# Performance work log

Hardware: AMD Instinct MI355X
Metric: run time of the kernel (lower is better)

Reference implementation:

```python
import jax, jax.numpy as jnp
import numpy as np

BLANK_ID = 0
B, MAX_T, MAX_U, VOCAB = 4, 200, 101, 1024  # MAX_U = max_label_len + 1


def setup_inputs() -> dict:
    key = jax.random.key(0)
    k1, k2, k3 = jax.random.split(key, 3)
    logits = jax.random.normal(k1, (B, MAX_T, MAX_U, VOCAB), dtype=jnp.float32)
    labels = jax.random.randint(k2, (B, MAX_U - 1), 0, VOCAB).astype(jnp.int64)
    label_lengths = jax.random.randint(k3, (B,), 1, MAX_U).astype(jnp.int64)  # in [1, MAX_U-1]
    attention_mask = jnp.ones((B, MAX_T), dtype=jnp.int32)
    return {"logits": logits, "labels": labels,
            "label_lengths": label_lengths, "attention_mask": attention_mask}


def _alpha_lattice(blank_lp, label_lp):
    """Forward variables for one sample.

    blank_lp: [T, U]   log P(blank | t, u)
    label_lp: [T, U-1] log P(y_u | t, u)  (label emitted at grid column u)
    Returns alpha [T, U], matching the reference recursion:
      alpha[0,0]   = blank_lp[0,0]
      alpha[t,0]   = alpha[t-1,0] + blank_lp[t,0]
      alpha[0,u]   = alpha[0,u-1] + label_lp[0,u-1]
      alpha[t,u]   = logaddexp(alpha[t-1,u]+blank_lp[t,u], alpha[t,u-1]+label_lp[t,u-1])
    """
    # First row: pure label path (cumulative sum along u).
    row0 = blank_lp[0, 0] + jnp.concatenate(
        [jnp.zeros((1,), blank_lp.dtype), jnp.cumsum(label_lp[0])])

    def time_step(prev_row, xs):
        b_t, l_t = xs                 # [U], [U-1]
        from_blank = prev_row + b_t   # blank transition into row t

        def u_step(carry, x):
            bl, lb = x
            a = jnp.logaddexp(bl, carry + lb)
            return a, a

        _, rest = jax.lax.scan(u_step, from_blank[0], (from_blank[1:], l_t))
        row = jnp.concatenate([from_blank[:1], rest])
        return row, row

    _, rows = jax.lax.scan(time_step, row0, (blank_lp[1:], label_lp[1:]))
    return jnp.concatenate([row0[None], rows], axis=0)  # [T, U]


def reference(logits, labels, label_lengths, attention_mask):
    Bn, maxT, maxU, V = logits.shape
    input_lengths = jnp.clip(attention_mask.sum(axis=1).astype(jnp.int32), 1, maxT)
    lab_lens = jnp.clip(label_lengths.astype(jnp.int32), 0, maxU - 1)
    labels_c = jnp.clip(labels, 0, V - 1)

    lp = jax.nn.log_softmax(logits, axis=-1)          # [B, T, U, V]
    blank_lp = lp[..., BLANK_ID]                      # [B, T, U]
    # label_lp[b, t, u] = lp[b, t, u, labels[b, u]] for u in [0, U-2]
    idx = jnp.broadcast_to(labels_c[:, None, :, None], (Bn, maxT, maxU - 1, 1))
    label_lp = jnp.take_along_axis(lp[:, :, :-1, :], idx, axis=3)[..., 0]

    alpha = jax.vmap(_alpha_lattice)(blank_lp, label_lp)  # [B, T, U]

    t_idx = input_lengths - 1
    u_idx = lab_lens                                  # U_b - 1 = label_len
    loss_b = -alpha[jnp.arange(Bn), t_idx, u_idx]

    valid = (input_lengths > 0) & (lab_lens > 0)
    loss_b = jnp.where(valid, loss_b, 0.0)
    num_valid = jnp.maximum(valid.sum(), 1)
    return loss_b.sum() / num_valid                   # reduction='mean'
```

## Files before the change

### kernel.cpp

```cpp
#include <hip/hip_runtime.h>
#include <hip/hip_bf16.h>
#include <math.h>

#define BB 4
#define TT 200
#define UU 101
#define VV 1024
#define NCELL (BB*TT*UU)

__device__ __forceinline__ float f4max(const float4& v) {
    return fmaxf(fmaxf(v.x, v.y), fmaxf(v.z, v.w));
}
__device__ __forceinline__ float f4comp(const float4& v, int c) {
    switch (c & 3) { case 0: return v.x; case 1: return v.y; case 2: return v.z; default: return v.w; }
}

__global__ __launch_bounds__(256) void lse_kernel(
        const float* __restrict__ logits,
        const int*   __restrict__ labels,
        float* __restrict__ blank_lp,
        float* __restrict__ label_lp) {
    const int wave = threadIdx.x >> 6;
    const int lane = threadIdx.x & 63;
    const int cell = blockIdx.x * 4 + wave;
    if (cell >= NCELL) return;
    const int b   = cell / (TT * UU);
    const int rem = cell % (TT * UU);
    const int t   = rem / UU;
    const int u   = rem % UU;

    const float4* src = (const float4*)(logits + (size_t)cell * VV);
    float4 x0 = src[lane];
    float4 x1 = src[lane + 64];
    float4 x2 = src[lane + 128];
    float4 x3 = src[lane + 192];

    float m = fmaxf(fmaxf(f4max(x0), f4max(x1)), fmaxf(f4max(x2), f4max(x3)));
    #pragma unroll
    for (int off = 32; off; off >>= 1) m = fmaxf(m, __shfl_xor(m, off));

    float s = 0.f;
    s += __expf(x0.x - m) + __expf(x0.y - m) + __expf(x0.z - m) + __expf(x0.w - m);
    s += __expf(x1.x - m) + __expf(x1.y - m) + __expf(x1.z - m) + __expf(x1.w - m);
    s += __expf(x2.x - m) + __expf(x2.y - m) + __expf(x2.z - m) + __expf(x2.w - m);
    s += __expf(x3.x - m) + __expf(x3.y - m) + __expf(x3.z - m) + __expf(x3.w - m);
    #pragma unroll
    for (int off = 32; off; off >>= 1) s += __shfl_xor(s, off);

    const float lse = m + __logf(s);

    if (lane == 0) blank_lp[cell] = x0.x - lse;

    if (u < UU - 1) {
        int l = labels[b * (UU - 1) + u];
        l = min(max(l, 0), VV - 1);
        const int lane_l = (l >> 2) & 63;
        if (lane == lane_l) {
            const int j = l >> 8;
            const int c = l & 3;
            float val = (j == 0) ? f4comp(x0, c) : (j == 1) ? f4comp(x1, c)
                      : (j == 2) ? f4comp(x2, c) : f4comp(x3, c);
            label_lp[(b * TT + t) * (UU - 1) + u] = val - lse;
        }
    }
}

__global__ __launch_bounds__(128) void alpha_kernel(
        const float* __restrict__ blank_lp,
        const float* __restrict__ label_lp,
        const int*   __restrict__ lab_lens,
        const int*   __restrict__ attn,
        float* __restrict__ loss_b,
        int*   __restrict__ valid_b) {
    const int b = blockIdx.x;
    const int u = threadIdx.x;

    __shared__ float buf[2][UU];
    __shared__ int   s_part[2];
    __shared__ float s_loss;

    int acc = 0;
    for (int i = threadIdx.x; i < TT; i += 128) acc += attn[b * TT + i];
    #pragma unroll
    for (int off = 32; off; off >>= 1) acc += __shfl_xor(acc, off);
    if ((threadIdx.x & 63) == 0) s_part[threadIdx.x >> 6] = acc;
    __syncthreads();
    int inlen = s_part[0] + s_part[1];
    inlen = min(max(inlen, 1), TT);
    const int tmax = inlen - 1;
    int lab = lab_lens[b];
    lab = min(max(lab, 0), UU - 1);
    const int ndiag = tmax + lab + 1;

    const float* bl_base = blank_lp + b * TT * UU;
    const float* lb_base = label_lp + b * TT * (UU - 1);
    const int um = min(u, UU - 1);
    const int ul = (um >= 1) ? (um - 1) : 0;

    auto fetch = [&](int d, float& fb, float& fl) {
        int tc = d - u;
        tc = min(max(tc, 0), TT - 1);
        fb = bl_base[tc * UU + um];
        fl = lb_base[tc * (UU - 1) + ul];
    };

    float cb[4], cl[4], nb[4], nl[4];
    #pragma unroll
    for (int k = 0; k < 4; ++k) fetch(k, cb[k], cl[k]);

    const int ng = (ndiag + 3) >> 2;
    for (int g = 0; g < ng; ++g) {
        const int dbase = g * 4;
        #pragma unroll
        for (int k = 0; k < 4; ++k) fetch(dbase + 4 + k, nb[k], nl[k]);
        #pragma unroll
        for (int k = 0; k < 4; ++k) {
            const int d = dbase + k;
            if (d < ndiag) {
                const int t = d - u;
                const bool act = (u <= lab) && (t >= 0) && (t <= tmax);
                if (act) {
                    const float fb = cb[k], fl = cl[k];
                    float v;
                    if (d == 0) {
                        v = fb;
                    } else if (u == 0) {
                        v = buf[(d - 1) & 1][0] + fb;
                    } else if (t == 0) {
                        v = buf[(d - 1) & 1][u - 1] + fl;
                    } else {
                        const float a = buf[(d - 1) & 1][u] + fb;
                        const float c = buf[(d - 1) & 1][u - 1] + fl;
                        const float mx = fmaxf(a, c), mn = fminf(a, c);
                        v = mx + log1pf(__expf(mn - mx));
                    }
                    buf[d & 1][u] = v;
                    if (t == tmax && u == lab) s_loss = -v;
                }
            }
            __syncthreads();
        }
        #pragma unroll
        for (int k = 0; k < 4; ++k) { cb[k] = nb[k]; cl[k] = nl[k]; }
    }

    if (threadIdx.x == 0) {
        loss_b[b]  = s_loss;
        valid_b[b] = (lab > 0) ? 1 : 0;
    }
}

__global__ void finalize_kernel(const float* __restrict__ loss_b,
                                const int* __restrict__ valid_b,
                                float* __restrict__ out) {
    if (threadIdx.x == 0 && blockIdx.x == 0) {
        float s = 0.f;
        int nv = 0;
        for (int b = 0; b < BB; ++b) {
            if (valid_b[b]) { s += loss_b[b]; ++nv; }
        }
        out[0] = s / (float)max(nv, 1);
    }
}

extern "C" void kernel_launch(void* const* d_in, const int* in_sizes, int n_in,
                              void* d_out, int out_size, void* d_ws, size_t ws_size,
                              hipStream_t stream) {
    const float* logits   = (const float*)d_in[0];
    const int*   labels   = (const int*)d_in[1];
    const int*   lab_lens = (const int*)d_in[2];
    const int*   attn     = (const int*)d_in[3];

    float* ws      = (float*)d_ws;
    float* blank   = ws;
    float* label   = blank + BB * TT * UU;
    float* loss_b  = label + BB * TT * (UU - 1);
    int*   valid_b = (int*)(loss_b + BB);

    lse_kernel<<<(NCELL + 3) / 4, 256, 0, stream>>>(logits, labels, blank, label);
    alpha_kernel<<<BB, 128, 0, stream>>>(blank, label, lab_lens, attn, loss_b, valid_b);
    finalize_kernel<<<1, 64, 0, stream>>>(loss_b, valid_b, (float*)d_out);
}
```

Measured before the change: 551.2 us.

## Skip log-softmax beyond label length and run alpha recursion per-wave with shuffles

The LSE kernel now exits early for cells with u greater than the sample's label length, so logits in unused lattice columns are never read. The alpha kernel maps each batch item to one 64-lane wave holding two u columns per lane. It passes neighbour values with shuffles instead of shared memory and block-wide barriers, and it folds the finalize reduction into the same kernel. The cost is a register-resident lattice and lanes that carry two columns each, plus relying on lab_lens to bound valid work.

Measured after the change: 636.8 us. +15.5%, slower.

```diff
diff --git a/kernel.cpp b/kernel.cpp
--- a/kernel.cpp
+++ b/kernel.cpp
@@ -1,5 +1,4 @@
 #include <hip/hip_runtime.h>
-#include <hip/hip_bf16.h>
 #include <math.h>
 
 #define BB 4
@@ -18,6 +17,7 @@
 __global__ __launch_bounds__(256) void lse_kernel(
         const float* __restrict__ logits,
         const int*   __restrict__ labels,
+        const int*   __restrict__ lab_lens,
         float* __restrict__ blank_lp,
         float* __restrict__ label_lp) {
     const int wave = threadIdx.x >> 6;
@@ -28,6 +28,10 @@
     const int rem = cell % (TT * UU);
     const int t   = rem / UU;
     const int u   = rem % UU;
+
+    int lab = lab_lens[b];
+    lab = min(max(lab, 0), UU - 1);
+    if (u > lab) return;
 
     const float4* src = (const float4*)(logits + (size_t)cell * VV);
     float4 x0 = src[lane];
@@ -51,7 +55,7 @@
 
     if (lane == 0) blank_lp[cell] = x0.x - lse;
 
-    if (u < UU - 1) {
+    if (u < lab) {
         int l = labels[b * (UU - 1) + u];
         l = min(max(l, 0), VV - 1);
         const int lane_l = (l >> 2) & 63;
@@ -65,100 +69,96 @@
     }
 }
 
-__global__ __launch_bounds__(128) void alpha_kernel(
+__global__ __launch_bounds__(256) void alpha_kernel(
         const float* __restrict__ blank_lp,
         const float* __restrict__ label_lp,
         const int*   __restrict__ lab_lens,
         const int*   __restrict__ attn,
-        float* __restrict__ loss_b,
-        int*   __restrict__ valid_b) {
-    const int b = blockIdx.x;
-    const int u = threadIdx.x;
-
-    __shared__ float buf[2][UU];
-    __shared__ int   s_part[2];
-    __shared__ float s_loss;
+        float* __restrict__ out) {
+    const int b    = threadIdx.x >> 6;
+    const int lane = threadIdx.x & 63;
 
     int acc = 0;
-    for (int i = threadIdx.x; i < TT; i += 128) acc += attn[b * TT + i];
+    for (int i = lane; i < TT; i += 64) acc += attn[b * TT + i];
     #pragma unroll
     for (int off = 32; off; off >>= 1) acc += __shfl_xor(acc, off);
-    if ((threadIdx.x & 63) == 0) s_part[threadIdx.x >> 6] = acc;
-    __syncthreads();
-    int inlen = s_part[0] + s_part[1];
-    inlen = min(max(inlen, 1), TT);
+    int inlen = min(max(acc, 1), TT);
     const int tmax = inlen - 1;
     int lab = lab_lens[b];
     lab = min(max(lab, 0), UU - 1);
     const int ndiag = tmax + lab + 1;
 
-    const float* bl_base = blank_lp + b * TT * UU;
-    const float* lb_base = label_lp + b * TT * (UU - 1);
-    const int um = min(u, UU - 1);
-    const int ul = (um >= 1) ? (um - 1) : 0;
+    const float* bl = blank_lp + b * TT * UU;
+    const float* lb = label_lp + b * TT * (UU - 1);
 
-    auto fetch = [&](int d, float& fb, float& fl) {
-        int tc = d - u;
-        tc = min(max(tc, 0), TT - 1);
-        fb = bl_base[tc * UU + um];
-        fl = lb_base[tc * (UU - 1) + ul];
+    const int u0 = lane * 2, u1 = u0 + 1;
+    const int c0 = min(u0, UU - 1), c1 = min(u1, UU - 1);
+    const int e0 = min(max(u0 - 1, 0), UU - 2), e1 = min(u1 - 1, UU - 2);
+
+    auto fetch = [&](int d, float& fb0, float& fl0, float& fb1, float& fl1) {
+        int t0 = min(max(d - u0, 0), TT - 1);
+        int t1 = min(max(d - u1, 0), TT - 1);
+        fb0 = bl[t0 * UU + c0];
+        fl0 = lb[t0 * (UU - 1) + e0];
+        fb1 = bl[t1 * UU + c1];
+        fl1 = lb[t1 * (UU - 1) + e1];
     };
 
-    float cb[4], cl[4], nb[4], nl[4];
+    float a0 = -INFINITY, a1 = -INFINITY;
+
+    float cb0[4], cl0[4], cb1[4], cl1[4];
+    float nb0[4], nl0[4], nb1[4], nl1[4];
     #pragma unroll
-    for (int k = 0; k < 4; ++k) fetch(k, cb[k], cl[k]);
+    for (int k = 0; k < 4; ++k) fetch(k, cb0[k], cl0[k], cb1[k], cl1[k]);
 
     const int ng = (ndiag + 3) >> 2;
     for (int g = 0; g < ng; ++g) {
         const int dbase = g * 4;
         #pragma unroll
-        for (int k = 0; k < 4; ++k) fetch(dbase + 4 + k, nb[k], nl[k]);
+        for (int k = 0; k < 4; ++k) fetch(dbase + 4 + k, nb0[k], nl0[k], nb1[k], nl1[k]);
         #pragma unroll
         for (int k = 0; k < 4; ++k) {
             const int d = dbase + k;
             if (d < ndiag) {
-                const int t = d - u;
-                const bool act = (u <= lab) && (t >= 0) && (t <= tmax);
-                if (act) {
-                    const float fb = cb[k], fl = cl[k];
-                    float v;
-                    if (d == 0) {
-                        v = fb;
-                    } else if (u == 0) {
-                        v = buf[(d - 1) & 1][0] + fb;
-                    } else if (t == 0) {
-                        v = buf[(d - 1) & 1][u - 1] + fl;
-                    } else {
-                        const float a = buf[(d - 1) & 1][u] + fb;
-                        const float c = buf[(d - 1) & 1][u - 1] + fl;
-                        const float mx = fmaxf(a, c), mn = fminf(a, c);
-                        v = mx + log1pf(__expf(mn - mx));
+                const float left = __shfl_up(a1, 1);
+                const int t0 = d - u0;
+                const int t1 = d - u1;
+                float v0 = a0, v1 = a1;
+                if (u0 <= lab && t0 >= 0 && t0 <= tmax) {
+                    if (d == 0)        v0 = cb0[k];
+                    else if (u0 == 0)  v0 = a0 + cb0[k];
+                    else if (t0 == 0)  v0 = left + cl0[k];
+                    else {
+                        const float x = a0 + cb0[k], y = left + cl0[k];
+                        const float mx = fmaxf(x, y), mn = fminf(x, y);
+                        v0 = mx + __logf(1.f + __expf(mn - mx));
                     }
-                    buf[d & 1][u] = v;
-                    if (t == tmax && u == lab) s_loss = -v;
                 }
+                if (u1 <= lab && t1 >= 0 && t1 <= tmax) {
+                    if (t1 == 0)       v1 = a0 + cl1[k];
+                    else {
+                        const float x = a1 + cb1[k], y = a0 + cl1[k];
+                        const float mx = fmaxf(x, y), mn = fminf(x, y);
+                        v1 = mx + __logf(1.f + __expf(mn - mx));
+                    }
+                }
+                a0 = v0; a1 = v1;
             }
-            __syncthreads();
         }
         #pragma unroll
-        for (int k = 0; k < 4; ++k) { cb[k] = nb[k]; cl[k] = nl[k]; }
+        for (int k = 0; k < 4; ++k) { cb0[k] = nb0[k]; cl0[k] = nl0[k];
+                                      cb1[k] = nb1[k]; cl1[k] = nl1[k]; }
     }
 
+    __shared__ float s_loss[BB];
+    __shared__ int   s_valid[BB];
+    if (u0 == lab) s_loss[b] = -a0;
+    if (u1 == lab) s_loss[b] = -a1;
+    if (lane == 0) s_valid[b] = (lab > 0) ? 1 : 0;
+    __syncthreads();
     if (threadIdx.x == 0) {
-        loss_b[b]  = s_loss;
-        valid_b[b] = (lab > 0) ? 1 : 0;
-    }
-}
-
-__global__ void finalize_kernel(const float* __restrict__ loss_b,
-                                const int* __restrict__ valid_b,
-                                float* __restrict__ out) {
-    if (threadIdx.x == 0 && blockIdx.x == 0) {
-        float s = 0.f;
-        int nv = 0;
-        for (int b = 0; b < BB; ++b) {
-            if (valid_b[b]) { s += loss_b[b]; ++nv; }
-        }
+        float s = 0.f; int nv = 0;
+        for (int i = 0; i < BB; ++i) if (s_valid[i]) { s += s_loss[i]; ++nv; }
         out[0] = s / (float)max(nv, 1);
     }
 }
@@ -171,13 +171,10 @@
     const int*   lab_lens = (const int*)d_in[2];
     const int*   attn     = (const int*)d_in[3];
 
-    float* ws      = (float*)d_ws;
-    float* blank   = ws;
-    float* label   = blank + BB * TT * UU;
-    float* loss_b  = label + BB * TT * (UU - 1);
-    int*   valid_b = (int*)(loss_b + BB);
+    float* ws    = (float*)d_ws;
+    float* blank = ws;
+    float* label = blank + BB * TT * UU;
 
-    lse_kernel<<<(NCELL + 3) / 4, 256, 0, stream>>>(logits, labels, blank, label);
-    alpha_kernel<<<BB, 128, 0, stream>>>(blank, label, lab_lens, attn, loss_b, valid_b);
-    finalize_kernel<<<1, 64, 0, stream>>>(loss_b, valid_b, (float*)d_out);
+    lse_kernel<<<(NCELL + 3) / 4, 256, 0, stream>>>(logits, labels, lab_lens, blank, label);
+    alpha_kernel<<<1, 256, 0, stream>>>(blank, label, lab_lens, attn, (float*)d_out);
 }
```

## Skip unused lattice cells and run alpha recursion in a single wave

Applied to the files above, without the earlier changes.

The log-softmax kernel now exits early for grid columns beyond each sample's label length, so logits rows that can never reach the final alpha cell are not read. The alpha kernel first stages the whole blank/label log-prob lattice into padded shared memory. It then runs the anti-diagonal recursion inside one 64-lane wave, each lane holding two columns and passing neighbour values with shuffles, which removes the per-diagonal block barrier. This depends on large dynamic shared memory, and it trades global-memory reads for a serial staging phase.

After: 473.7 us. 14.1% less time.

```diff
diff --git a/kernel.cpp b/kernel.cpp
--- a/kernel.cpp
+++ b/kernel.cpp
@@ -1,5 +1,4 @@
 #include <hip/hip_runtime.h>
-#include <hip/hip_bf16.h>
 #include <math.h>
 
 #define BB 4
@@ -7,6 +6,7 @@
 #define UU 101
 #define VV 1024
 #define NCELL (BB*TT*UU)
+#define PAD 102
 
 __device__ __forceinline__ float f4max(const float4& v) {
     return fmaxf(fmaxf(v.x, v.y), fmaxf(v.z, v.w));
@@ -18,6 +18,7 @@
 __global__ __launch_bounds__(256) void lse_kernel(
         const float* __restrict__ logits,
         const int*   __restrict__ labels,
+        const int*   __restrict__ lab_lens,
         float* __restrict__ blank_lp,
         float* __restrict__ label_lp) {
     const int wave = threadIdx.x >> 6;
@@ -29,6 +30,10 @@
     const int t   = rem / UU;
     const int u   = rem % UU;
 
+    int lab = lab_lens[b];
+    lab = min(max(lab, 0), UU - 1);
+    if (u > lab) return;
+
     const float4* src = (const float4*)(logits + (size_t)cell * VV);
     float4 x0 = src[lane];
     float4 x1 = src[lane + 64];
@@ -51,7 +56,7 @@
 
     if (lane == 0) blank_lp[cell] = x0.x - lse;
 
-    if (u < UU - 1) {
+    if (u < lab) {
         int l = labels[b * (UU - 1) + u];
         l = min(max(l, 0), VV - 1);
         const int lane_l = (l >> 2) & 63;
@@ -65,87 +70,114 @@
     }
 }
 
-__global__ __launch_bounds__(128) void alpha_kernel(
+__global__ __launch_bounds__(256) void alpha_kernel(
         const float* __restrict__ blank_lp,
         const float* __restrict__ label_lp,
         const int*   __restrict__ lab_lens,
         const int*   __restrict__ attn,
         float* __restrict__ loss_b,
         int*   __restrict__ valid_b) {
-    const int b = blockIdx.x;
-    const int u = threadIdx.x;
-
-    __shared__ float buf[2][UU];
-    __shared__ int   s_part[2];
-    __shared__ float s_loss;
+    const int b    = blockIdx.x;
+    const int tid  = threadIdx.x;
+    const int lane = tid & 63;
+
+    extern __shared__ float smem[];
+    float* bs = smem;
+    float* ls = smem + TT * PAD;
+
+    const float* bl = blank_lp + b * TT * UU;
+    const float* lb = label_lp + b * TT * (UU - 1);
+
+    for (int i = tid; i < TT * UU; i += 256) {
+        int t = i / UU, u = i - t * UU;
+        bs[t * PAD + u] = bl[i];
+    }
+    for (int i = tid; i < TT * (UU - 1); i += 256) {
+        int t = i / (UU - 1), u = i - t * (UU - 1);
+        ls[t * PAD + u] = lb[i];
+    }
 
     int acc = 0;
-    for (int i = threadIdx.x; i < TT; i += 128) acc += attn[b * TT + i];
+    for (int i = lane; i < TT; i += 64) acc += attn[b * TT + i];
     #pragma unroll
     for (int off = 32; off; off >>= 1) acc += __shfl_xor(acc, off);
-    if ((threadIdx.x & 63) == 0) s_part[threadIdx.x >> 6] = acc;
-    __syncthreads();
-    int inlen = s_part[0] + s_part[1];
-    inlen = min(max(inlen, 1), TT);
-    const int tmax = inlen - 1;
+    const int tmax = min(max(acc, 1), TT) - 1;
     int lab = lab_lens[b];
     lab = min(max(lab, 0), UU - 1);
     const int ndiag = tmax + lab + 1;
 
-    const float* bl_base = blank_lp + b * TT * UU;
-    const float* lb_base = label_lp + b * TT * (UU - 1);
-    const int um = min(u, UU - 1);
-    const int ul = (um >= 1) ? (um - 1) : 0;
-
-    auto fetch = [&](int d, float& fb, float& fl) {
-        int tc = d - u;
-        tc = min(max(tc, 0), TT - 1);
-        fb = bl_base[tc * UU + um];
-        fl = lb_base[tc * (UU - 1) + ul];
+    __syncthreads();
+    if (tid >= 64) return;
+
+    const int uA  = lane;
+    const int uB  = lane + 64;
+    const int uBc = min(uB, UU - 1);
+    const int eA  = max(uA - 1, 0);
+    const int eB  = uBc - 1;
+
+    auto fetch = [&](int d, float& fbA, float& flA, float& fbB, float& flB) {
+        int tA = min(max(d - uA, 0), TT - 1);
+        int tB = min(max(d - uB, 0), TT - 1);
+        fbA = bs[tA * PAD + uA];
+        flA = ls[tA * PAD + eA];
+        fbB = bs[tB * PAD + uBc];
+        flB = ls[tB * PAD + eB];
     };
 
-    float cb[4], cl[4], nb[4], nl[4];
-    #pragma unroll
-    for (int k = 0; k < 4; ++k) fetch(k, cb[k], cl[k]);
+    float aA = -INFINITY, aB = -INFINITY;
+
+    float cbA[4], clA[4], cbB[4], clB[4];
+    float nbA[4], nlA[4], nbB[4], nlB[4];
+    #pragma unroll
+    for (int k = 0; k < 4; ++k) fetch(k, cbA[k], clA[k], cbB[k], clB[k]);
 
     const int ng = (ndiag + 3) >> 2;
     for (int g = 0; g < ng; ++g) {
         const int dbase = g * 4;
         #pragma unroll
-        for (int k = 0; k < 4; ++k) fetch(dbase + 4 + k, nb[k], nl[k]);
+        for (int k = 0; k < 4; ++k) fetch(dbase + 4 + k, nbA[k], nlA[k], nbB[k], nlB[k]);
         #pragma unroll
         for (int k = 0; k < 4; ++k) {
             const int d = dbase + k;
             if (d < ndiag) {
-                const int t = d - u;
-                const bool act = (u <= lab) && (t >= 0) && (t <= tmax);
-                if (act) {
-                    const float fb = cb[k], fl = cl[k];
-                    float v;
-                    if (d == 0) {
-                        v = fb;
-                    } else if (u == 0) {
-                        v = buf[(d - 1) & 1][0] + fb;
-                    } else if (t == 0) {
-                        v = buf[(d - 1) & 1][u - 1] + fl;
-                    } else {
-                        const float a = buf[(d - 1) & 1][u] + fb;
-                        const float c = buf[(d - 1) & 1][u - 1] + fl;
-                        const float mx = fmaxf(a, c), mn = fminf(a, c);
-                        v = mx + log1pf(__expf(mn - mx));
-                    }
-                    buf[d & 1][u] = v;
-                    if (t == tmax && u == lab) s_loss = -v;
+                const float leftA = __shfl_up(aA, 1);
+                const float upB   = __shfl_up(aB, 1);
+                const float wrapB = __shfl(aA, 63);
+                const float leftB = (lane == 0) ? wrapB : upB;
+                const int tA = d - uA;
+                const int tB = d - uB;
+                {
+                    const float x  = aA + cbA[k];
+                    const float y  = leftA + clA[k];
+                    const float mx = fmaxf(x, y), mn = fminf(x, y);
+                    const float full = mx + __logf(1.f + __expf(mn - mx));
+                    const float v = (d == 0) ? cbA[k]
+                                  : (uA == 0) ? x
+                                  : (tA == 0) ? y
+                                  : full;
+                    const bool act = (uA <= lab) && (tA >= 0) && (tA <= tmax);
+                    aA = act ? v : aA;
+                }
+                {
+                    const float x  = aB + cbB[k];
+                    const float y  = leftB + clB[k];
+                    const float mx = fmaxf(x, y), mn = fminf(x, y);
+                    const float full = mx + __logf(1.f + __expf(mn - mx));
+                    const float v = (tB == 0) ? y : full;
+                    const bool act = (uB <= lab) && (tB >= 0) && (tB <= tmax);
+                    aB = act ? v : aB;
                 }
             }
-            __syncthreads();
         }
         #pragma unroll
-        for (int k = 0; k < 4; ++k) { cb[k] = nb[k]; cl[k] = nl[k]; }
-    }
-
-    if (threadIdx.x == 0) {
-        loss_b[b]  = s_loss;
+        for (int k = 0; k < 4; ++k) { cbA[k] = nbA[k]; clA[k] = nlA[k];
+                                      cbB[k] = nbB[k]; clB[k] = nlB[k]; }
+    }
+
+    const float cand = (lab >= 64) ? aB : aA;
+    const float v = __shfl(cand, lab & 63);
+    if (lane == 0) {
+        loss_b[b]  = -v;
         valid_b[b] = (lab > 0) ? 1 : 0;
     }
 }
@@ -177,7 +209,16 @@
     float* loss_b  = label + BB * TT * (UU - 1);
     int*   valid_b = (int*)(loss_b + BB);
 
-    lse_kernel<<<(NCELL + 3) / 4, 256, 0, stream>>>(logits, labels, blank, label);
-    alpha_kernel<<<BB, 128, 0, stream>>>(blank, label, lab_lens, attn, loss_b, valid_b);
+    static bool attr_set = false;
+    if (!attr_set) {
+        hipFuncSetAttribute((const void*)alpha_kernel,
+                            hipFuncAttributeMaxDynamicSharedMemorySize,
+                            2 * TT * PAD * (int)sizeof(float));
+        attr_set = true;
+    }
+
+    lse_kernel<<<(NCELL + 3) / 4, 256, 0, stream>>>(logits, labels, lab_lens, blank, label);
+    alpha_kernel<<<BB, 256, 2 * TT * PAD * sizeof(float), stream>>>(
+        blank, label, lab_lens, attn, loss_b, valid_b);
     finalize_kernel<<<1, 64, 0, stream>>>(loss_b, valid_b, (float*)d_out);
 }
```
